# Optimization experiments

Measured on AMD Instinct MI355X. Metric: run time of the kernel, lower is better.

The kernel has to match this reference:

```python
import jax, jax.numpy as jnp
import numpy as np

B, N, IN_DIM, OUT_DIM, K = 64, 256, 512, 512, 8
DK = OUT_DIM // K  # per-kernel feature dim


def setup_inputs() -> dict:
    key = jax.random.key(0)
    k1, k2, k3, k4 = jax.random.split(key, 4)
    node_feats = jax.random.normal(k1, (B, N, IN_DIM), dtype=jnp.float32)
    adj = jax.random.uniform(k2, (B, K, N, N), dtype=jnp.float32)
    weight = jax.random.normal(k3, (IN_DIM, OUT_DIM), dtype=jnp.float32) * (1.0 / np.sqrt(IN_DIM))
    bias = jax.random.normal(k4, (OUT_DIM,), dtype=jnp.float32) * 0.01
    return {"node_feats": node_feats, "adj": adj, "weight": weight, "bias": bias}


def reference(node_feats, adj, weight, bias):
    # kernel linear + ReLU: (b, n, out_dim)
    h = jax.nn.relu(jnp.einsum('bni,io->bno', node_feats, weight) + bias)
    # split into kernel slots: (b, n, k, dk)
    h = h.reshape(B, N, K, DK)
    # graph.aggregate: per-kernel dense message passing over adjacency
    # out[b,n,k,d] = sum_m adj[b,k,n,m] * h[b,m,k,d]
    agg = jnp.einsum('bknm,bmkd->bnkd', adj, h)
    return agg.reshape(B, N, OUT_DIM)
```

## Files before the change

kernel.cpp:

```cpp
#include <hip/hip_runtime.h>
#include <hip/hip_bf16.h>


typedef __attribute__((ext_vector_type(8))) short short8;
typedef __attribute__((ext_vector_type(4))) float floatx4;

__device__ __forceinline__ unsigned short f2bf(float f) {
    union { float f; unsigned u; } v; v.f = f;
    unsigned r = v.u + 0x7FFFu + ((v.u >> 16) & 1u);
    return (unsigned short)(r >> 16);
}

__device__ __forceinline__ unsigned pk2bf(float a, float b) {
    union { __hip_bfloat162 h; unsigned u; } cv;
    cv.h = __float22bfloat162_rn(make_float2(a, b));
    return cv.u;
}

__global__ __launch_bounds__(256) void wt_kernel(const float* __restrict__ W,
                                                 unsigned short* __restrict__ Wt) {
    __shared__ unsigned short t_lds[64 * 66];
    const int tile = blockIdx.x;
    const int k0 = (tile >> 3) * 64;
    const int o0 = (tile & 7) * 64;
    const int t = threadIdx.x;
    const int c = t & 63;
    const int rb = t >> 6;
#pragma unroll
    for (int i = 0; i < 16; ++i) {
        int r = i * 4 + rb;
        t_lds[c * 66 + r] = f2bf(W[(size_t)(k0 + r) * 512 + o0 + c]);
    }
    __syncthreads();
#pragma unroll
    for (int i = 0; i < 16; ++i) {
        int o_r = i * 4 + rb;
        Wt[(size_t)(o0 + o_r) * 512 + k0 + c] = t_lds[o_r * 66 + c];
    }
}

__global__ __launch_bounds__(1024, 8) void fused_kernel(
    const float* __restrict__ X, const unsigned short* __restrict__ Wt,
    const float* __restrict__ bias, const float* __restrict__ adj,
    float* __restrict__ out) {
    __shared__ union {
        struct {
            unsigned short a[256 * 40];
            unsigned short w[64 * 40];
        } s1;
        struct {
            unsigned short ht[64 * 256];
            unsigned short at[64 * 256];
        } s2;
    } lds;

    const int id = blockIdx.x;
    const int b = id & 63;
    const int ks = id >> 6;

    const int tid = threadIdx.x;
    const int lane = tid & 63, w = tid >> 6;
    const int lrow = lane & 15, quad = lane >> 4;

    const float* Xb = X + (size_t)b * 256 * 512;
    const unsigned short* Wslice = Wt + (size_t)ks * 64 * 512;

    floatx4 acc1[4];
    const floatx4 fzero = {0.f, 0.f, 0.f, 0.f};
#pragma unroll
    for (int j = 0; j < 4; ++j) acc1[j] = fzero;

    for (int kb = 0; kb < 16; ++kb) {
        const int k0 = kb * 32;
#pragma unroll
        for (int i = 0; i < 2; ++i) {
            int c4 = tid + i * 1024;
            int rr = c4 >> 3;
            int cc = (c4 & 7) * 4;
            const float4 v = *(const float4*)(Xb + (size_t)rr * 512 + k0 + cc);
            unsigned p01 = pk2bf(v.x, v.y);
            unsigned p23 = pk2bf(v.z, v.w);
            unsigned* dst = (unsigned*)(lds.s1.a + rr * 40 + cc);
            dst[0] = p01; dst[1] = p23;
        }
        if (tid < 512) {
            int rr = tid >> 3;
            int cc = (tid & 7) * 4;
            *(ushort4*)(lds.s1.w + rr * 40 + cc) =
                *(const ushort4*)(Wslice + (size_t)rr * 512 + k0 + cc);
        }
        __syncthreads();

        short8 af, bfr[4];
        af = *(const short8*)(lds.s1.a + (w * 16 + lrow) * 40 + quad * 8);
#pragma unroll
        for (int j = 0; j < 4; ++j)
            bfr[j] = *(const short8*)(lds.s1.w + (16 * j + lrow) * 40 + quad * 8);
#pragma unroll
        for (int j = 0; j < 4; ++j)
            acc1[j] = __builtin_amdgcn_mfma_f32_16x16x32_bf16(af, bfr[j], acc1[j], 0, 0, 0);
        __syncthreads();
    }

#pragma unroll
    for (int j = 0; j < 4; ++j) {
        int d = 16 * j + lrow;
        float bv = bias[ks * 64 + d];
        int m = w * 16 + quad * 4;
        floatx4 c = acc1[j];
        unsigned p01 = pk2bf(fmaxf(c.x + bv, 0.f), fmaxf(c.y + bv, 0.f));
        unsigned p23 = pk2bf(fmaxf(c.z + bv, 0.f), fmaxf(c.w + bv, 0.f));
        int jm = 2 * w + (quad >> 1);
        int phys = jm ^ (d & 7);
        unsigned* d32 = (unsigned*)(lds.s2.ht + d * 256 + phys * 8 + (quad & 1) * 4);
        d32[0] = p01; d32[1] = p23;
    }
    __syncthreads();

    const float* Abase = adj + ((size_t)(b * 8 + ks)) * 65536;
    const int wn = w & 3, wd = w >> 2;

    for (int nt = 0; nt < 4; ++nt) {
#pragma unroll
        for (int s = 0; s < 2; ++s) {
            int c = s * 1024 + tid;
            int nl = c >> 5;
            int jm = c & 31;
            const float* src = Abase + ((size_t)(nt * 64 + nl)) * 256 + jm * 8;
            float4 v0 = *(const float4*)src;
            float4 v1 = *(const float4*)(src + 4);
            union { short8 sh; unsigned u[4]; } t;
            t.u[0] = pk2bf(v0.x, v0.y);
            t.u[1] = pk2bf(v0.z, v0.w);
            t.u[2] = pk2bf(v1.x, v1.y);
            t.u[3] = pk2bf(v1.z, v1.w);
            *(short8*)(lds.s2.at + nl * 256 + ((jm ^ (nl & 7)) * 8)) = t.sh;
        }
        __syncthreads();

        floatx4 acc = fzero;
        const int nl = wn * 16 + lrow;
        const int d  = wd * 16 + lrow;
#pragma unroll
        for (int mt = 0; mt < 8; ++mt) {
            int jm = 4 * mt + quad;
            short8 afr = *(const short8*)(lds.s2.at + nl * 256 + ((jm ^ (lrow & 7)) * 8));
            short8 bfr = *(const short8*)(lds.s2.ht + d  * 256 + ((jm ^ (lrow & 7)) * 8));
            acc = __builtin_amdgcn_mfma_f32_16x16x32_bf16(afr, bfr, acc, 0, 0, 0);
        }
        __syncthreads();

        int n_g = nt * 64 + wn * 16 + quad * 4;
        float* dst = out + ((size_t)b * 256 + n_g) * 512 + ks * 64 + wd * 16 + lrow;
        dst[0 * 512] = acc.x;
        dst[1 * 512] = acc.y;
        dst[2 * 512] = acc.z;
        dst[3 * 512] = acc.w;
    }
}

extern "C" void kernel_launch(void* const* d_in, const int* in_sizes, int n_in,
                              void* d_out, int out_size, void* d_ws, size_t ws_size,
                              hipStream_t stream) {
    const float* X    = (const float*)d_in[0];
    const float* adj  = (const float*)d_in[1];
    const float* W    = (const float*)d_in[2];
    const float* bias = (const float*)d_in[3];
    float* out = (float*)d_out;

    unsigned short* Wt = (unsigned short*)d_ws;

    wt_kernel<<<64, 256, 0, stream>>>(W, Wt);
    fused_kernel<<<512, 1024, 0, stream>>>(X, Wt, bias, adj, out);
}
```

Baseline: 250.3 us.

## Load MFMA operands directly from global memory, dropping LDS staging

Both phases now load their MFMA A-fragments (and the W fragments in phase 1) straight from global memory into registers. Before, X, W and adj tiles were staged through LDS with barriers around each step. In phase 2 each wave now owns 16 full node rows and accumulates all four 16-wide feature tiles, replacing the 4-iteration node-tile loop with its LDS writes and syncs. This removes most barriers and shrinks LDS to the h tile only. The cost is uncoalesced, strided per-lane global reads, which rely on cache to hide latency.

```diff
diff --git a/kernel.cpp b/kernel.cpp
--- a/kernel.cpp
+++ b/kernel.cpp
@@ -43,16 +43,7 @@
     const float* __restrict__ X, const unsigned short* __restrict__ Wt,
     const float* __restrict__ bias, const float* __restrict__ adj,
     float* __restrict__ out) {
-    __shared__ union {
-        struct {
-            unsigned short a[256 * 40];
-            unsigned short w[64 * 40];
-        } s1;
-        struct {
-            unsigned short ht[64 * 256];
-            unsigned short at[64 * 256];
-        } s2;
-    } lds;
+    __shared__ unsigned short ht[64 * 256];
 
     const int id = blockIdx.x;
     const int b = id & 63;
@@ -70,92 +61,74 @@
 #pragma unroll
     for (int j = 0; j < 4; ++j) acc1[j] = fzero;
 
+    const float* xrow = Xb + (size_t)(w * 16 + lrow) * 512 + quad * 8;
+    const unsigned short* wrow = Wslice + (size_t)lrow * 512 + quad * 8;
+
+#pragma unroll 2
     for (int kb = 0; kb < 16; ++kb) {
         const int k0 = kb * 32;
+        float4 xa = *(const float4*)(xrow + k0);
+        float4 xc = *(const float4*)(xrow + k0 + 4);
+        union { short8 s; unsigned u[4]; } af;
+        af.u[0] = pk2bf(xa.x, xa.y);
+        af.u[1] = pk2bf(xa.z, xa.w);
+        af.u[2] = pk2bf(xc.x, xc.y);
+        af.u[3] = pk2bf(xc.z, xc.w);
 #pragma unroll
-        for (int i = 0; i < 2; ++i) {
-            int c4 = tid + i * 1024;
-            int rr = c4 >> 3;
-            int cc = (c4 & 7) * 4;
-            const float4 v = *(const float4*)(Xb + (size_t)rr * 512 + k0 + cc);
-            unsigned p01 = pk2bf(v.x, v.y);
-            unsigned p23 = pk2bf(v.z, v.w);
-            unsigned* dst = (unsigned*)(lds.s1.a + rr * 40 + cc);
-            dst[0] = p01; dst[1] = p23;
+        for (int j = 0; j < 4; ++j) {
+            short8 bfr = *(const short8*)(wrow + (size_t)j * 16 * 512 + k0);
+            acc1[j] = __builtin_amdgcn_mfma_f32_16x16x32_bf16(af.s, bfr, acc1[j], 0, 0, 0);
         }
-        if (tid < 512) {
-            int rr = tid >> 3;
-            int cc = (tid & 7) * 4;
-            *(ushort4*)(lds.s1.w + rr * 40 + cc) =
-                *(const ushort4*)(Wslice + (size_t)rr * 512 + k0 + cc);
-        }
-        __syncthreads();
-
-        short8 af, bfr[4];
-        af = *(const short8*)(lds.s1.a + (w * 16 + lrow) * 40 + quad * 8);
-#pragma unroll
-        for (int j = 0; j < 4; ++j)
-            bfr[j] = *(const short8*)(lds.s1.w + (16 * j + lrow) * 40 + quad * 8);
-#pragma unroll
-        for (int j = 0; j < 4; ++j)
-            acc1[j] = __builtin_amdgcn_mfma_f32_16x16x32_bf16(af, bfr[j], acc1[j], 0, 0, 0);
-        __syncthreads();
     }
 
 #pragma unroll
     for (int j = 0; j < 4; ++j) {
         int d = 16 * j + lrow;
         float bv = bias[ks * 64 + d];
-        int m = w * 16 + quad * 4;
         floatx4 c = acc1[j];
         unsigned p01 = pk2bf(fmaxf(c.x + bv, 0.f), fmaxf(c.y + bv, 0.f));
         unsigned p23 = pk2bf(fmaxf(c.z + bv, 0.f), fmaxf(c.w + bv, 0.f));
         int jm = 2 * w + (quad >> 1);
         int phys = jm ^ (d & 7);
-        unsigned* d32 = (unsigned*)(lds.s2.ht + d * 256 + phys * 8 + (quad & 1) * 4);
+        unsigned* d32 = (unsigned*)(ht + d * 256 + phys * 8 + (quad & 1) * 4);
         d32[0] = p01; d32[1] = p23;
     }
     __syncthreads();
 
     const float* Abase = adj + ((size_t)(b * 8 + ks)) * 65536;
-    const int wn = w & 3, wd = w >> 2;
+    const float* arow = Abase + (size_t)(w * 16 + lrow) * 256 + quad * 8;
 
-    for (int nt = 0; nt < 4; ++nt) {
+    floatx4 acc[4];
 #pragma unroll
-        for (int s = 0; s < 2; ++s) {
-            int c = s * 1024 + tid;
-            int nl = c >> 5;
-            int jm = c & 31;
-            const float* src = Abase + ((size_t)(nt * 64 + nl)) * 256 + jm * 8;
-            float4 v0 = *(const float4*)src;
-            float4 v1 = *(const float4*)(src + 4);
-            union { short8 sh; unsigned u[4]; } t;
-            t.u[0] = pk2bf(v0.x, v0.y);
-            t.u[1] = pk2bf(v0.z, v0.w);
-            t.u[2] = pk2bf(v1.x, v1.y);
-            t.u[3] = pk2bf(v1.z, v1.w);
-            *(short8*)(lds.s2.at + nl * 256 + ((jm ^ (nl & 7)) * 8)) = t.sh;
+    for (int j = 0; j < 4; ++j) acc[j] = fzero;
+
+#pragma unroll 2
+    for (int mt = 0; mt < 8; ++mt) {
+        float4 a0 = *(const float4*)(arow + mt * 32);
+        float4 a1 = *(const float4*)(arow + mt * 32 + 4);
+        union { short8 s; unsigned u[4]; } afr;
+        afr.u[0] = pk2bf(a0.x, a0.y);
+        afr.u[1] = pk2bf(a0.z, a0.w);
+        afr.u[2] = pk2bf(a1.x, a1.y);
+        afr.u[3] = pk2bf(a1.z, a1.w);
+        const int jm = 4 * mt + quad;
+#pragma unroll
+        for (int dt = 0; dt < 4; ++dt) {
+            int d = dt * 16 + lrow;
+            short8 bfr = *(const short8*)(ht + d * 256 + ((jm ^ (d & 7)) * 8));
+            acc[dt] = __builtin_amdgcn_mfma_f32_16x16x32_bf16(afr.s, bfr, acc[dt], 0, 0, 0);
         }
-        __syncthreads();
+    }
 
-        floatx4 acc = fzero;
-        const int nl = wn * 16 + lrow;
-        const int d  = wd * 16 + lrow;
+    const int n_g = w * 16 + quad * 4;
+    float* dst = out + ((size_t)b * 256 + n_g) * 512 + ks * 64 + lrow;
 #pragma unroll
-        for (int mt = 0; mt < 8; ++mt) {
-            int jm = 4 * mt + quad;
-            short8 afr = *(const short8*)(lds.s2.at + nl * 256 + ((jm ^ (lrow & 7)) * 8));
-            short8 bfr = *(const short8*)(lds.s2.ht + d  * 256 + ((jm ^ (lrow & 7)) * 8));
-            acc = __builtin_amdgcn_mfma_f32_16x16x32_bf16(afr, bfr, acc, 0, 0, 0);
-        }
-        __syncthreads();
-
-        int n_g = nt * 64 + wn * 16 + quad * 4;
-        float* dst = out + ((size_t)b * 256 + n_g) * 512 + ks * 64 + wd * 16 + lrow;
-        dst[0 * 512] = acc.x;
-        dst[1 * 512] = acc.y;
-        dst[2 * 512] = acc.z;
-        dst[3 * 512] = acc.w;
+    for (int dt = 0; dt < 4; ++dt) {
+        float* p = dst + dt * 16;
+        p[0 * 512] = acc[dt].x;
+        p[1 * 512] = acc[dt].y;
+        p[2 * 512] = acc[dt].z;
+        p[3 * 512] = acc[dt].w;
     }
 }
 
```

Result: slower. 305.6 us (+22.1%).
